# Kernel optimization log

Hardware: AMD Instinct MI355X
Metric: run time of the kernel (lower is better)

Reference implementation:

```python
import jax, jax.numpy as jnp
import numpy as np

WAY, SHOT, HEADS = 5, 5, 12
DIM, L = 768, 512
HD = DIM // HEADS  # 64
SCALE = 1.0 / (HD ** 0.5)


def _layernorm(x, g, b, eps=1e-5):
    m = jnp.mean(x, axis=-1, keepdims=True)
    v = jnp.var(x, axis=-1, keepdims=True)
    return (x - m) / jnp.sqrt(v + eps) * g + b


def setup_inputs() -> dict:
    key = jax.random.key(0)
    ks = jax.random.split(key, 7)
    x = jax.random.normal(ks[0], (WAY * SHOT, L, DIM), dtype=jnp.float32)
    Wq = 0.02 * jax.random.normal(ks[1], (DIM, DIM), dtype=jnp.float32)
    Wk = 0.02 * jax.random.normal(ks[2], (DIM, DIM), dtype=jnp.float32)
    Wv = 0.02 * jax.random.normal(ks[3], (DIM, DIM), dtype=jnp.float32)
    Wo = 0.02 * jax.random.normal(ks[4], (DIM, DIM), dtype=jnp.float32)
    wp = 0.02 * jax.random.normal(ks[5], (DIM,), dtype=jnp.float32)
    return {
        "x": x,
        "Wq": Wq, "bq": jnp.zeros((DIM,), jnp.float32),
        "Wk": Wk, "bk": jnp.zeros((DIM,), jnp.float32),
        "Wv": Wv, "bv": jnp.zeros((DIM,), jnp.float32),
        "gamma": jnp.ones((DIM,), jnp.float32),
        "beta": jnp.zeros((DIM,), jnp.float32),
        "wp": wp, "bp": jnp.zeros((), jnp.float32),
        "Wo": Wo, "bo": jnp.zeros((DIM,), jnp.float32),
    }


def reference(x, Wq, bq, Wk, bk, Wv, bv, gamma, beta, wp, bp, Wo, bo):
    # flag == 'XS' branch; mask=None; dropout in eval mode (identity).
    x = x.reshape(WAY, SHOT, L, DIM)
    # projections -> (way, heads, shot, l, head_dim)
    q = (x @ Wq.T + bq).reshape(WAY, SHOT, L, HEADS, HD).transpose(0, 3, 1, 2, 4)
    k = (x @ Wk.T + bk).reshape(WAY, SHOT, L, HEADS, HD).transpose(0, 3, 1, 2, 4)
    v = (x @ Wv.T + bv).reshape(WAY, SHOT, L, HEADS, HD).transpose(0, 3, 1, 2, 4)

    # branch 1: standard token attention, scores (w,h,s,l,l)
    s1 = jnp.einsum('whsld,whsmd->whslm', q, k) * SCALE
    w1 = jax.nn.softmax(s1, axis=-1)
    o1 = jnp.einsum('whslm,whsmd->whsld', w1, v)
    o1 = o1.transpose(0, 2, 3, 1, 4).reshape(WAY, SHOT, L, DIM)  # (w,s,l,h*d)
    a1 = jnp.max(o1, axis=2)  # max-pool over tokens -> (w,s,dim)

    # branch 2: transposed 'channel' attention across shots, scores (w,h,d,s,s)
    s2 = jnp.einsum('whsld,whtld->whdst', q, k) * SCALE
    w2 = jax.nn.softmax(s2, axis=-1)
    o2 = jnp.einsum('whdst,whtld->whdsl', w2, v)
    o2 = o2.transpose(0, 3, 4, 1, 2).reshape(WAY, SHOT, L, DIM)  # (w,s,l,h*d)
    a2 = jnp.max(o2, axis=2)  # (w,s,dim)

    attn = (_layernorm(a1, gamma, beta) + _layernorm(a2, gamma, beta)) * 0.5
    proto = jnp.tanh(attn)
    pw = jax.nn.softmax(proto @ wp + bp, axis=-1)[..., None]  # softmax over shots
    proto = pw * attn
    proto = proto @ Wo.T + bo
    return jnp.sum(proto, axis=1)  # (way, dim)
```

## Files before the change

kernel.cpp:

```cpp
#include <hip/hip_runtime.h>
#include <math.h>

#define WAY 5
#define SHOT 5
#define HEADS 12
#define DIM 768
#define LSEQ 512
#define HD 64
#define NROWS (WAY*SHOT*LSEQ)
#define SCALE 0.125f
#define NXEL ((size_t)NROWS*DIM)
#define NWEL ((size_t)DIM*DIM)

typedef __attribute__((ext_vector_type(8))) short short8;
typedef __attribute__((ext_vector_type(4))) float f32x4;
typedef __attribute__((ext_vector_type(4))) unsigned short ushort4v;

__device__ __forceinline__ float bf2f(unsigned short u) {
    union { unsigned int i; float f; } x; x.i = ((unsigned int)u) << 16; return x.f;
}
__device__ __forceinline__ unsigned short f2bf(float f) {
    union { float f; unsigned int i; } x; x.f = f;
    unsigned int r = x.i + 0x7FFFu + ((x.i >> 16) & 1u);
    return (unsigned short)(r >> 16);
}

#define NX4 (NROWS*DIM/4)
#define NW4 (DIM*DIM/4)
__global__ __launch_bounds__(256) void cast_all(
    const float* __restrict__ X, const float* __restrict__ Wq,
    const float* __restrict__ Wk, const float* __restrict__ Wv,
    unsigned short* __restrict__ Xb, unsigned short* __restrict__ Wb)
{
    int i = blockIdx.x * 256 + threadIdx.x;
    const float* s; unsigned short* d; int off;
    if (i < NX4)               { s = X;  d = Xb;            off = i; }
    else if (i < NX4 + NW4)    { s = Wq; d = Wb;            off = i - NX4; }
    else if (i < NX4 + 2*NW4)  { s = Wk; d = Wb + NWEL;     off = i - NX4 - NW4; }
    else if (i < NX4 + 3*NW4)  { s = Wv; d = Wb + 2*NWEL;   off = i - NX4 - 2*NW4; }
    else return;
    float4 f = ((const float4*)s)[off];
    ushort4v o;
    o.x = f2bf(f.x); o.y = f2bf(f.y); o.z = f2bf(f.z); o.w = f2bf(f.w);
    *(ushort4v*)(d + (size_t)off*4) = o;
}

__global__ __launch_bounds__(256) void qkv_mfma(
    const unsigned short* __restrict__ Xb, const unsigned short* __restrict__ Wball,
    const float* __restrict__ bq, const float* __restrict__ bk, const float* __restrict__ bv,
    unsigned short* __restrict__ qkv_out)
{
    const int bid  = blockIdx.x;
    const int sw   = (bid & 7) * 225 + (bid >> 3);
    const int mblk = sw / 18;
    const int nblk = sw - mblk * 18;
    const int m0   = mblk * 128;
    const int n0g  = nblk * 128;
    const int which = n0g / DIM;
    const int n0    = n0g - which * DIM;

    const unsigned short* W = Wball + (size_t)n0g * DIM;
    const float* bias = (which == 0) ? bq : ((which == 1) ? bk : bv);
    unsigned short* out = qkv_out + (size_t)which * NXEL;

    __shared__ __align__(16) unsigned short Ab[128*64];
    __shared__ __align__(16) unsigned short Bb[128*64];

    const int t = threadIdx.x;
    const int w = t >> 6;
    const int lane = t & 63;
    const int quad = lane >> 4;
    const int l15 = lane & 15;
    const int wm = (w & 1) * 64;
    const int wn = (w >> 1) * 64;

    const int srow   = lane >> 3;
    const int gchunk = (lane & 7) ^ srow;

    f32x4 acc[4][4];
    #pragma unroll
    for (int i = 0; i < 4; i++)
        #pragma unroll
        for (int j = 0; j < 4; j++)
            acc[i][j] = (f32x4){0.f, 0.f, 0.f, 0.f};

    for (int k0 = 0; k0 < DIM; k0 += 64) {
        #pragma unroll
        for (int c = 0; c < 4; c++) {
            const int lrow = w*32 + c*8;
            const unsigned short* gA = Xb + (size_t)(m0 + lrow + srow)*DIM + k0 + gchunk*8;
            const unsigned short* gB = W  + (size_t)(lrow + srow)*DIM      + k0 + gchunk*8;
            __builtin_amdgcn_global_load_lds(
                (const __attribute__((address_space(1))) unsigned int*)gA,
                (__attribute__((address_space(3))) unsigned int*)&Ab[lrow*64], 16, 0, 0);
            __builtin_amdgcn_global_load_lds(
                (const __attribute__((address_space(1))) unsigned int*)gB,
                (__attribute__((address_space(3))) unsigned int*)&Bb[lrow*64], 16, 0, 0);
        }
        __syncthreads();

        #pragma unroll
        for (int kk = 0; kk < 2; kk++) {
            const int ch = kk*4 + quad;
            short8 af[4], bf_[4];
            #pragma unroll
            for (int i = 0; i < 4; i++) {
                const int row = wm + i*16 + l15;
                af[i]  = *(const short8*)&Ab[row*64 + ((ch ^ (row & 7)) << 3)];
            }
            #pragma unroll
            for (int j = 0; j < 4; j++) {
                const int row = wn + j*16 + l15;
                bf_[j] = *(const short8*)&Bb[row*64 + ((ch ^ (row & 7)) << 3)];
            }
            #pragma unroll
            for (int i = 0; i < 4; i++)
                #pragma unroll
                for (int j = 0; j < 4; j++)
                    acc[i][j] = __builtin_amdgcn_mfma_f32_16x16x32_bf16(af[i], bf_[j], acc[i][j], 0, 0, 0);
        }
        __syncthreads();
    }

    #pragma unroll
    for (int j = 0; j < 4; j++) {
        const int col = n0 + wn + j*16 + l15;
        const float bv_ = bias[col];
        #pragma unroll
        for (int i = 0; i < 4; i++) {
            #pragma unroll
            for (int r = 0; r < 4; r++) {
                const int row = m0 + wm + i*16 + quad*4 + r;
                out[(size_t)row*DIM + col] = f2bf(acc[i][j][r] + bv_);
            }
        }
    }
}

__device__ __forceinline__ int swz(int row, int u) {
    return row*64 + ((u ^ (row & 7)) << 3);
}

__global__ __launch_bounds__(256) void attn1_mfma(
    const unsigned short* __restrict__ qb, const unsigned short* __restrict__ kb,
    const unsigned short* __restrict__ vb, float* __restrict__ a1p)
{
    int whs = blockIdx.x;
    const int chunk = blockIdx.y;
    const int si = whs % SHOT;  whs /= SHOT;
    const int hi = whs % HEADS; whs /= HEADS;
    const int wi = whs;
    const size_t baseRow = (size_t)(wi*SHOT + si) * LSEQ;
    const int colBase = hi * HD;

    __shared__ __align__(16) unsigned short Qs[64*64];
    __shared__ __align__(16) unsigned short Ks[64*64];
    __shared__ __align__(16) unsigned short Vt[64*64];
    __shared__ __align__(16) unsigned short Pb[64*64];
    __shared__ float cmaxs[4][64];

    const int t = threadIdx.x;
    const int w = t >> 6;
    const int lane = t & 63;
    const int quad = lane >> 4;
    const int l15 = lane & 15;

    #pragma unroll
    for (int p = 0; p < 2; p++) {
        int idx = p*256 + t;
        int row = idx >> 3, u = idx & 7;
        *(short8*)&Qs[swz(row, u)] =
            *(const short8*)&qb[(baseRow + chunk*64 + row)*DIM + colBase + u*8];
    }

    float l_part[4] = {0.f, 0.f, 0.f, 0.f};
    f32x4 o_acc[4];
    #pragma unroll
    for (int d = 0; d < 4; d++) o_acc[d] = (f32x4){0.f, 0.f, 0.f, 0.f};

    for (int kt = 0; kt < 8; kt++) {
        __syncthreads();
        #pragma unroll
        for (int p = 0; p < 2; p++) {
            int idx = p*256 + t;
            int row = idx >> 3, u = idx & 7;
            *(short8*)&Ks[swz(row, u)] =
                *(const short8*)&kb[(baseRow + kt*64 + row)*DIM + colBase + u*8];
        }
        #pragma unroll
        for (int p = 0; p < 2; p++) {
            int idx = p*256 + t;
            int d = idx & 63, lc = idx >> 6;
            unsigned short tmp[8];
            #pragma unroll
            for (int jj = 0; jj < 8; jj++)
                tmp[jj] = vb[(baseRow + kt*64 + lc*8 + jj)*DIM + colBase + d];
            *(short8*)&Vt[swz(d, lc)] = *(const short8*)tmp;
        }
        __syncthreads();

        f32x4 s_acc[4];
        #pragma unroll
        for (int nt = 0; nt < 4; nt++) s_acc[nt] = (f32x4){0.f, 0.f, 0.f, 0.f};
        short8 aq[2];
        #pragma unroll
        for (int kk = 0; kk < 2; kk++)
            aq[kk] = *(const short8*)&Qs[swz(w*16 + l15, kk*4 + quad)];
        #pragma unroll
        for (int kk = 0; kk < 2; kk++) {
            #pragma unroll
            for (int nt = 0; nt < 4; nt++) {
                short8 bk_ = *(const short8*)&Ks[swz(nt*16 + l15, kk*4 + quad)];
                s_acc[nt] = __builtin_amdgcn_mfma_f32_16x16x32_bf16(aq[kk], bk_, s_acc[nt], 0, 0, 0);
            }
        }

        #pragma unroll
        for (int nt = 0; nt < 4; nt++) {
            #pragma unroll
            for (int r = 0; r < 4; r++) {
                float e = __expf(s_acc[nt][r] * SCALE);
                s_acc[nt][r] = e;
                l_part[r] += e;
            }
        }

        #pragma unroll
        for (int nt = 0; nt < 4; nt++) {
            int ucol = nt*2 + (l15 >> 3);
            int cofs = l15 & 7;
            #pragma unroll
            for (int r = 0; r < 4; r++) {
                int row = w*16 + quad*4 + r;
                Pb[swz(row, ucol) + cofs] = f2bf(s_acc[nt][r]);
            }
        }

        short8 ap[2];
        #pragma unroll
        for (int kk = 0; kk < 2; kk++)
            ap[kk] = *(const short8*)&Pb[swz(w*16 + l15, kk*4 + quad)];
        #pragma unroll
        for (int kk = 0; kk < 2; kk++) {
            #pragma unroll
            for (int dt = 0; dt < 4; dt++) {
                short8 bv_ = *(const short8*)&Vt[swz(dt*16 + l15, kk*4 + quad)];
                o_acc[dt] = __builtin_amdgcn_mfma_f32_16x16x32_bf16(ap[kk], bv_, o_acc[dt], 0, 0, 0);
            }
        }
    }

    float l_tot[4];
    #pragma unroll
    for (int r = 0; r < 4; r++) {
        float s = l_part[r];
        #pragma unroll
        for (int off = 1; off < 16; off <<= 1) s += __shfl_xor(s, off);
        l_tot[r] = s;
    }

    float cm[4];
    #pragma unroll
    for (int dt = 0; dt < 4; dt++) {
        float mx = -1e30f;
        #pragma unroll
        for (int r = 0; r < 4; r++) mx = fmaxf(mx, o_acc[dt][r] / l_tot[r]);
        mx = fmaxf(mx, __shfl_xor(mx, 16));
        mx = fmaxf(mx, __shfl_xor(mx, 32));
        cm[dt] = mx;
    }
    if (quad == 0) {
        #pragma unroll
        for (int dt = 0; dt < 4; dt++) cmaxs[w][dt*16 + l15] = cm[dt];
    }
    __syncthreads();
    if (t < 64) {
        float mx = fmaxf(fmaxf(cmaxs[0][t], cmaxs[1][t]), fmaxf(cmaxs[2][t], cmaxs[3][t]));
        a1p[((size_t)((wi*HEADS + hi)*SHOT + si)*8 + chunk)*64 + t] = mx;
    }
}

__global__ __launch_bounds__(256) void attn2_scores(
    const unsigned short* __restrict__ qb, const unsigned short* __restrict__ kb,
    float* __restrict__ P1)
{
    const int wh = blockIdx.x, ch = blockIdx.y;
    const int wi = wh / HEADS, hi = wh % HEADS;
    const int t = threadIdx.x;
    const int doct = t & 7;
    const int pr = t >> 3;
    if (pr >= 25) return;
    const int si = pr / 5, tt = pr % 5;
    const int colB = hi*HD + doct*8;

    const unsigned short* qrow = qb + ((size_t)(wi*SHOT+si)*LSEQ + ch*64)*DIM + colB;
    const unsigned short* krow = kb + ((size_t)(wi*SHOT+tt)*LSEQ + ch*64)*DIM + colB;

    float acc[8] = {};
    for (int l = 0; l < 64; l++) {
        short8 q8 = *(const short8*)(qrow + (size_t)l*DIM);
        short8 k8 = *(const short8*)(krow + (size_t)l*DIM);
        #pragma unroll
        for (int j = 0; j < 8; j++)
            acc[j] += bf2f((unsigned short)q8[j]) * bf2f((unsigned short)k8[j]);
    }
    #pragma unroll
    for (int j = 0; j < 8; j++)
        P1[((size_t)(wh*25 + pr)*64 + doct*8 + j)*8 + ch] = acc[j];
}

__global__ __launch_bounds__(320) void attn2_pmax(
    const float* __restrict__ P1, const unsigned short* __restrict__ vb,
    float* __restrict__ P2)
{
    const int wh = blockIdx.x, ch = blockIdx.y;
    const int wi = wh / HEADS, hi = wh % HEADS;
    const int t = threadIdx.x;
    const int si = t / 64;
    const int r  = t & 63;
    const int doct = r >> 3, lsub = r & 7;

    __shared__ float ssc[SHOT*SHOT*HD];

    for (int e = t; e < SHOT*SHOT*HD; e += 320) {
        const float* p = P1 + (size_t)(wh*25)*64*8 + (size_t)e*8;
        float s = 0.f;
        #pragma unroll
        for (int c = 0; c < 8; c++) s += p[c];
        ssc[e] = s * SCALE;
    }
    __syncthreads();

    float wgt[SHOT][8];
    #pragma unroll
    for (int j = 0; j < 8; j++) {
        const int d = doct*8 + j;
        float sum = 0.f;
        #pragma unroll
        for (int tt = 0; tt < SHOT; tt++) {
            float e = __expf(ssc[(si*SHOT + tt)*HD + d]);
            wgt[tt][j] = e; sum += e;
        }
        const float inv = 1.f / sum;
        #pragma unroll
        for (int tt = 0; tt < SHOT; tt++) wgt[tt][j] *= inv;
    }

    const int colB = hi*HD + doct*8;
    float m[8];
    #pragma unroll
    for (int j = 0; j < 8; j++) m[j] = -1e30f;

    for (int lc = 0; lc < 8; lc++) {
        const int l = ch*64 + lsub*8 + lc;
        float val[8] = {};
        #pragma unroll
        for (int tt = 0; tt < SHOT; tt++) {
            short8 v8 = *(const short8*)(vb + ((size_t)(wi*SHOT+tt)*LSEQ + l)*DIM + colB);
            #pragma unroll
            for (int j = 0; j < 8; j++)
                val[j] += wgt[tt][j] * bf2f((unsigned short)v8[j]);
        }
        #pragma unroll
        for (int j = 0; j < 8; j++) m[j] = fmaxf(m[j], val[j]);
    }

    #pragma unroll
    for (int off = 1; off < 8; off <<= 1)
        #pragma unroll
        for (int j = 0; j < 8; j++) m[j] = fmaxf(m[j], __shfl_xor(m[j], off));

    if (lsub == 0) {
        #pragma unroll
        for (int j = 0; j < 8; j++)
            P2[((size_t)(wh*SHOT + si)*64 + doct*8 + j)*8 + ch] = m[j];
    }
}

__global__ __launch_bounds__(256) void combine(
    const float* __restrict__ a1p, const float* __restrict__ P2,
    const float* __restrict__ gamma, const float* __restrict__ beta,
    const float* __restrict__ wp, const float* __restrict__ bp,
    float* __restrict__ attn_ws, float* __restrict__ logits)
{
    const int wi = blockIdx.x / SHOT;
    const int si = blockIdx.x % SHOT;
    const int t  = threadIdx.x;

    __shared__ float row1[DIM];
    __shared__ float row2[DIM];
    __shared__ float rbuf[4][4];

    for (int j = t; j < DIM; j += 256) {
        int h = j / HD, d = j % HD;
        const float* p1 = a1p + ((size_t)((wi*HEADS + h)*SHOT + si) * 8) * 64 + d;
        float mx = -1e30f;
        #pragma unroll
        for (int c = 0; c < 8; c++) mx = fmaxf(mx, p1[c * 64]);
        row1[j] = mx;
        const float* p2 = P2 + ((size_t)((wi*HEADS + h)*SHOT + si)*64 + d)*8;
        float mx2 = -1e30f;
        #pragma unroll
        for (int c = 0; c < 8; c++) mx2 = fmaxf(mx2, p2[c]);
        row2[j] = mx2;
    }
    __syncthreads();

    float s1 = 0, q1 = 0, s2 = 0, q2 = 0;
    for (int j = t; j < DIM; j += 256) {
        float x1 = row1[j]; s1 += x1; q1 += x1*x1;
        float x2 = row2[j]; s2 += x2; q2 += x2*x2;
    }
    #pragma unroll
    for (int off = 32; off > 0; off >>= 1) {
        s1 += __shfl_down(s1, off); q1 += __shfl_down(q1, off);
        s2 += __shfl_down(s2, off); q2 += __shfl_down(q2, off);
    }
    const int wid = t / 64, lane = t % 64;
    if (lane == 0) { rbuf[wid][0] = s1; rbuf[wid][1] = q1; rbuf[wid][2] = s2; rbuf[wid][3] = q2; }
    __syncthreads();
    if (t == 0) {
        float a = 0, b = 0, c = 0, dd = 0;
        #pragma unroll
        for (int i = 0; i < 4; i++) { a += rbuf[i][0]; b += rbuf[i][1]; c += rbuf[i][2]; dd += rbuf[i][3]; }
        rbuf[0][0] = a; rbuf[0][1] = b; rbuf[0][2] = c; rbuf[0][3] = dd;
    }
    __syncthreads();
    const float mean1 = rbuf[0][0] / (float)DIM;
    const float var1  = rbuf[0][1] / (float)DIM - mean1*mean1;
    const float mean2 = rbuf[0][2] / (float)DIM;
    const float var2  = rbuf[0][3] / (float)DIM - mean2*mean2;
    const float inv1 = rsqrtf(var1 + 1e-5f);
    const float inv2 = rsqrtf(var2 + 1e-5f);

    float dotp = 0.0f;
    for (int j = t; j < DIM; j += 256) {
        float v1 = (row1[j] - mean1) * inv1 * gamma[j] + beta[j];
        float v2 = (row2[j] - mean2) * inv2 * gamma[j] + beta[j];
        float at = 0.5f * (v1 + v2);
        attn_ws[(size_t)(wi*SHOT + si) * DIM + j] = at;
        dotp += tanhf(at) * wp[j];
    }
    #pragma unroll
    for (int off = 32; off > 0; off >>= 1) dotp += __shfl_down(dotp, off);
    __syncthreads();
    if (lane == 0) rbuf[wid][0] = dotp;
    __syncthreads();
    if (t == 0)
        logits[wi*SHOT + si] = rbuf[0][0] + rbuf[1][0] + rbuf[2][0] + rbuf[3][0] + bp[0];
}

__global__ __launch_bounds__(256) void outproj(
    const float* __restrict__ attn_ws, const float* __restrict__ logits,
    const float* __restrict__ Wo, const float* __restrict__ bo,
    float* __restrict__ out)
{
    const int t = threadIdx.x;
    __shared__ __align__(16) float P[WAY][DIM];

    float swt[WAY][SHOT];
    #pragma unroll
    for (int w5 = 0; w5 < WAY; w5++) {
        float lg[SHOT];
        float mx = -1e30f;
        #pragma unroll
        for (int s = 0; s < SHOT; s++) { lg[s] = logits[w5*SHOT + s]; mx = fmaxf(mx, lg[s]); }
        float sum = 0.f;
        #pragma unroll
        for (int s = 0; s < SHOT; s++) { lg[s] = __expf(lg[s] - mx); sum += lg[s]; }
        const float inv = 1.f / sum;
        #pragma unroll
        for (int s = 0; s < SHOT; s++) swt[w5][s] = lg[s] * inv;
    }

    #pragma unroll
    for (int c = 0; c < 3; c++) {
        const int d = c*256 + t;
        #pragma unroll
        for (int w5 = 0; w5 < WAY; w5++) {
            float a = 0.f;
            #pragma unroll
            for (int s = 0; s < SHOT; s++)
                a += swt[w5][s] * attn_ws[(size_t)(w5*SHOT + s)*DIM + d];
            P[w5][d] = a;
        }
    }
    __syncthreads();

    const int wid = t >> 6, lane = t & 63;
    const int j = blockIdx.x * 4 + wid;

    float acc[WAY] = {0.f, 0.f, 0.f, 0.f, 0.f};
    #pragma unroll
    for (int c = 0; c < 3; c++) {
        const int d = c*256 + lane*4;
        const float4 wo = *(const float4*)&Wo[(size_t)j*DIM + d];
        #pragma unroll
        for (int w5 = 0; w5 < WAY; w5++) {
            const float4 p = *(const float4*)&P[w5][d];
            acc[w5] += p.x*wo.x + p.y*wo.y + p.z*wo.z + p.w*wo.w;
        }
    }
    #pragma unroll
    for (int off = 32; off > 0; off >>= 1)
        #pragma unroll
        for (int w5 = 0; w5 < WAY; w5++)
            acc[w5] += __shfl_down(acc[w5], off);

    if (lane == 0) {
        const float b5 = 5.0f * bo[j];
        #pragma unroll
        for (int w5 = 0; w5 < WAY; w5++)
            out[(size_t)w5*DIM + j] = acc[w5] + b5;
    }
}

extern "C" void kernel_launch(void* const* d_in, const int* in_sizes, int n_in,
                              void* d_out, int out_size, void* d_ws, size_t ws_size,
                              hipStream_t stream) {
    const float* X     = (const float*)d_in[0];
    const float* Wq    = (const float*)d_in[1];
    const float* bq    = (const float*)d_in[2];
    const float* Wk    = (const float*)d_in[3];
    const float* bk    = (const float*)d_in[4];
    const float* Wv    = (const float*)d_in[5];
    const float* bv    = (const float*)d_in[6];
    const float* gamma = (const float*)d_in[7];
    const float* beta  = (const float*)d_in[8];
    const float* wp    = (const float*)d_in[9];
    const float* bp    = (const float*)d_in[10];
    const float* Wo    = (const float*)d_in[11];
    const float* bo    = (const float*)d_in[12];
    float* out = (float*)d_out;

    unsigned short* Xb   = (unsigned short*)d_ws;
    unsigned short* Wb   = Xb + NXEL;
    unsigned short* qkvb = Wb + 3*NWEL;
    unsigned short* qb = qkvb;
    unsigned short* kb = qkvb + NXEL;
    unsigned short* vb = qkvb + 2*NXEL;

    float* a1p    = (float*)(qkvb + 3*NXEL);
    float* P1     = a1p + (size_t)WAY*HEADS*SHOT*8*64;
    float* P2     = P1 + (size_t)WAY*HEADS*SHOT*SHOT*64*8;
    float* attn_b = P2 + (size_t)WAY*HEADS*SHOT*64*8;
    float* logits = attn_b + (size_t)WAY*SHOT*DIM;

    const int castN = NX4 + 3*NW4;
    cast_all<<<(castN + 255)/256, 256, 0, stream>>>(X, Wq, Wk, Wv, Xb, Wb);

    qkv_mfma<<<1800, 256, 0, stream>>>(Xb, Wb, bq, bk, bv, qkvb);

    dim3 g2(WAY*HEADS*SHOT, 8);
    attn1_mfma<<<g2, 256, 0, stream>>>(qb, kb, vb, a1p);

    dim3 g3(WAY*HEADS, 8);
    attn2_scores<<<g3, 256, 0, stream>>>(qb, kb, P1);
    attn2_pmax<<<g3, 320, 0, stream>>>(P1, vb, P2);

    combine<<<WAY*SHOT, 256, 0, stream>>>(a1p, P2, gamma, beta, wp, bp, attn_b, logits);
    outproj<<<192, 256, 0, stream>>>(attn_b, logits, Wo, bo, out);
}
```

Before: 280.6 us.

## Enlarge QKV GEMM tiles to 256x256 with double-buffered LDS pipeline

```diff
diff --git a/kernel.cpp b/kernel.cpp
--- a/kernel.cpp
+++ b/kernel.cpp
@@ -45,93 +45,128 @@
     *(ushort4v*)(d + (size_t)off*4) = o;
 }
 
-__global__ __launch_bounds__(256) void qkv_mfma(
+__global__ __launch_bounds__(512, 2) void qkv_mfma(
     const unsigned short* __restrict__ Xb, const unsigned short* __restrict__ Wball,
     const float* __restrict__ bq, const float* __restrict__ bk, const float* __restrict__ bv,
     unsigned short* __restrict__ qkv_out)
 {
-    const int bid  = blockIdx.x;
-    const int sw   = (bid & 7) * 225 + (bid >> 3);
-    const int mblk = sw / 18;
-    const int nblk = sw - mblk * 18;
-    const int m0   = mblk * 128;
-    const int n0g  = nblk * 128;
-    const int which = n0g / DIM;
-    const int n0    = n0g - which * DIM;
-
-    const unsigned short* W = Wball + (size_t)n0g * DIM;
+    const int bid = blockIdx.x;
+    const int xcd = bid & 7;
+    const int loc = bid >> 3;
+    const int wgid = (xcd < 2 ? xcd*57 : 2*57 + (xcd-2)*56) + loc;
+    const int mblk = wgid / 9;
+    const int nblk = wgid % 9;
+    const int m0   = mblk * 256;
+    const int which = nblk / 3;
+    const int n0    = (nblk % 3) * 256;
+
+    const unsigned short* W = Wball + (size_t)(nblk * 256) * DIM;
     const float* bias = (which == 0) ? bq : ((which == 1) ? bk : bv);
     unsigned short* out = qkv_out + (size_t)which * NXEL;
 
-    __shared__ __align__(16) unsigned short Ab[128*64];
-    __shared__ __align__(16) unsigned short Bb[128*64];
+    __shared__ __align__(16) unsigned short Ab[2][256*64];
+    __shared__ __align__(16) unsigned short Bb[2][256*64];
 
     const int t = threadIdx.x;
     const int w = t >> 6;
     const int lane = t & 63;
     const int quad = lane >> 4;
     const int l15 = lane & 15;
-    const int wm = (w & 1) * 64;
-    const int wn = (w >> 1) * 64;
+    const int wm = w >> 2;
+    const int wn = w & 3;
 
     const int srow   = lane >> 3;
     const int gchunk = (lane & 7) ^ srow;
 
-    f32x4 acc[4][4];
-    #pragma unroll
-    for (int i = 0; i < 4; i++)
+    auto stage = [&](int kt, int buf) {
+        const int k0 = kt * 64;
+        #pragma unroll
+        for (int c = 0; c < 4; ++c) {
+            const int lrow = w*32 + c*8;
+            const unsigned short* gA = Xb + (size_t)(m0 + lrow + srow)*DIM + k0 + gchunk*8;
+            __builtin_amdgcn_global_load_lds(
+                (const __attribute__((address_space(1))) unsigned int*)gA,
+                (__attribute__((address_space(3))) unsigned int*)&Ab[buf][lrow*64], 16, 0, 0);
+            const unsigned short* gB = W + (size_t)(lrow + srow)*DIM + k0 + gchunk*8;
+            __builtin_amdgcn_global_load_lds(
+                (const __attribute__((address_space(1))) unsigned int*)gB,
+                (__attribute__((address_space(3))) unsigned int*)&Bb[buf][lrow*64], 16, 0, 0);
+        }
+    };
+
+    f32x4 acc[8][4];
+    #pragma unroll
+    for (int i = 0; i < 8; i++)
         #pragma unroll
         for (int j = 0; j < 4; j++)
             acc[i][j] = (f32x4){0.f, 0.f, 0.f, 0.f};
 
-    for (int k0 = 0; k0 < DIM; k0 += 64) {
-        #pragma unroll
-        for (int c = 0; c < 4; c++) {
-            const int lrow = w*32 + c*8;
-            const unsigned short* gA = Xb + (size_t)(m0 + lrow + srow)*DIM + k0 + gchunk*8;
-            const unsigned short* gB = W  + (size_t)(lrow + srow)*DIM      + k0 + gchunk*8;
-            __builtin_amdgcn_global_load_lds(
-                (const __attribute__((address_space(1))) unsigned int*)gA,
-                (__attribute__((address_space(3))) unsigned int*)&Ab[lrow*64], 16, 0, 0);
-            __builtin_amdgcn_global_load_lds(
-                (const __attribute__((address_space(1))) unsigned int*)gB,
-                (__attribute__((address_space(3))) unsigned int*)&Bb[lrow*64], 16, 0, 0);
-        }
-        __syncthreads();
-
-        #pragma unroll
-        for (int kk = 0; kk < 2; kk++) {
-            const int ch = kk*4 + quad;
-            short8 af[4], bf_[4];
-            #pragma unroll
-            for (int i = 0; i < 4; i++) {
-                const int row = wm + i*16 + l15;
-                af[i]  = *(const short8*)&Ab[row*64 + ((ch ^ (row & 7)) << 3)];
+    stage(0, 0);
+    stage(1, 1);
+    asm volatile("s_waitcnt vmcnt(8)" ::: "memory");
+    __builtin_amdgcn_s_barrier();
+
+    for (int kt = 0; kt < 12; ++kt) {
+        const unsigned short* As = &Ab[kt & 1][0];
+        const unsigned short* Bs = &Bb[kt & 1][0];
+
+        short8 bfr[4][2];
+        #pragma unroll
+        for (int nf = 0; nf < 4; ++nf)
+            #pragma unroll
+            for (int kk = 0; kk < 2; ++kk) {
+                const int row = wn*64 + nf*16 + l15;
+                const int ch  = kk*4 + quad;
+                bfr[nf][kk] = *(const short8*)&Bs[row*64 + ((ch ^ (row & 7)) << 3)];
             }
-            #pragma unroll
-            for (int j = 0; j < 4; j++) {
-                const int row = wn + j*16 + l15;
-                bf_[j] = *(const short8*)&Bb[row*64 + ((ch ^ (row & 7)) << 3)];
-            }
-            #pragma unroll
-            for (int i = 0; i < 4; i++)
+
+        #pragma unroll
+        for (int p = 0; p < 4; ++p) {
+            short8 afr[2][2];
+            #pragma unroll
+            for (int i = 0; i < 2; ++i)
                 #pragma unroll
-                for (int j = 0; j < 4; j++)
-                    acc[i][j] = __builtin_amdgcn_mfma_f32_16x16x32_bf16(af[i], bf_[j], acc[i][j], 0, 0, 0);
-        }
-        __syncthreads();
-    }
-
-    #pragma unroll
-    for (int j = 0; j < 4; j++) {
-        const int col = n0 + wn + j*16 + l15;
+                for (int kk = 0; kk < 2; ++kk) {
+                    const int row = wm*128 + (p*2 + i)*16 + l15;
+                    const int ch  = kk*4 + quad;
+                    afr[i][kk] = *(const short8*)&As[row*64 + ((ch ^ (row & 7)) << 3)];
+                }
+            __builtin_amdgcn_s_setprio(1);
+            #pragma unroll
+            for (int i = 0; i < 2; ++i)
+                #pragma unroll
+                for (int nf = 0; nf < 4; ++nf) {
+                    acc[p*2+i][nf] = __builtin_amdgcn_mfma_f32_16x16x32_bf16(
+                        afr[i][0], bfr[nf][0], acc[p*2+i][nf], 0, 0, 0);
+                    acc[p*2+i][nf] = __builtin_amdgcn_mfma_f32_16x16x32_bf16(
+                        afr[i][1], bfr[nf][1], acc[p*2+i][nf], 0, 0, 0);
+                }
+            __builtin_amdgcn_s_setprio(0);
+            if (p < 3) __builtin_amdgcn_s_barrier();
+        }
+
+        __builtin_amdgcn_sched_barrier(0);
+        __builtin_amdgcn_s_barrier();
+
+        if (kt + 2 < 12) {
+            stage(kt + 2, kt & 1);
+            asm volatile("s_waitcnt vmcnt(8)" ::: "memory");
+        } else {
+            asm volatile("s_waitcnt vmcnt(0)" ::: "memory");
+        }
+        __builtin_amdgcn_s_barrier();
+    }
+
+    #pragma unroll
+    for (int nf = 0; nf < 4; ++nf) {
+        const int col = n0 + wn*64 + nf*16 + l15;
         const float bv_ = bias[col];
         #pragma unroll
-        for (int i = 0; i < 4; i++) {
-            #pragma unroll
-            for (int r = 0; r < 4; r++) {
-                const int row = m0 + wm + i*16 + quad*4 + r;
-                out[(size_t)row*DIM + col] = f2bf(acc[i][j][r] + bv_);
+        for (int mf = 0; mf < 8; ++mf) {
+            #pragma unroll
+            for (int r = 0; r < 4; ++r) {
+                const int row = m0 + wm*128 + mf*16 + quad*4 + r;
+                out[(size_t)row*DIM + col] = f2bf(acc[mf][nf][r] + bv_);
             }
         }
     }
@@ -549,7 +584,7 @@
     const int castN = NX4 + 3*NW4;
     cast_all<<<(castN + 255)/256, 256, 0, stream>>>(X, Wq, Wk, Wv, Xb, Wb);
 
-    qkv_mfma<<<1800, 256, 0, stream>>>(Xb, Wb, bq, bk, bv, qkvb);
+    qkv_mfma<<<450, 512, 0, stream>>>(Xb, Wb, bq, bk, bv, qkvb);
 
     dim3 g2(WAY*HEADS*SHOT, 8);
     attn1_mfma<<<g2, 256, 0, stream>>>(qb, kb, vb, a1p);
```

Result: no change. 280.8 us (+0.1%).

## Double-buffer QKV GEMM LDS tiles and stage output through LDS

Applied to the files above, without the earlier changes.

```diff
diff --git a/kernel.cpp b/kernel.cpp
--- a/kernel.cpp
+++ b/kernel.cpp
@@ -63,8 +63,7 @@
     const float* bias = (which == 0) ? bq : ((which == 1) ? bk : bv);
     unsigned short* out = qkv_out + (size_t)which * NXEL;
 
-    __shared__ __align__(16) unsigned short Ab[128*64];
-    __shared__ __align__(16) unsigned short Bb[128*64];
+    __shared__ __align__(16) unsigned short Sm[4][128*64];
 
     const int t = threadIdx.x;
     const int w = t >> 6;
@@ -77,6 +76,9 @@
     const int srow   = lane >> 3;
     const int gchunk = (lane & 7) ^ srow;
 
+    const unsigned short* gAbase = Xb + (size_t)(m0 + w*32 + srow)*DIM + gchunk*8;
+    const unsigned short* gBbase = W  + (size_t)(w*32 + srow)*DIM      + gchunk*8;
+
     f32x4 acc[4][4];
     #pragma unroll
     for (int i = 0; i < 4; i++)
@@ -84,20 +86,32 @@
         for (int j = 0; j < 4; j++)
             acc[i][j] = (f32x4){0.f, 0.f, 0.f, 0.f};
 
-    for (int k0 = 0; k0 < DIM; k0 += 64) {
-        #pragma unroll
-        for (int c = 0; c < 4; c++) {
-            const int lrow = w*32 + c*8;
-            const unsigned short* gA = Xb + (size_t)(m0 + lrow + srow)*DIM + k0 + gchunk*8;
-            const unsigned short* gB = W  + (size_t)(lrow + srow)*DIM      + k0 + gchunk*8;
-            __builtin_amdgcn_global_load_lds(
-                (const __attribute__((address_space(1))) unsigned int*)gA,
-                (__attribute__((address_space(3))) unsigned int*)&Ab[lrow*64], 16, 0, 0);
-            __builtin_amdgcn_global_load_lds(
-                (const __attribute__((address_space(1))) unsigned int*)gB,
-                (__attribute__((address_space(3))) unsigned int*)&Bb[lrow*64], 16, 0, 0);
-        }
-        __syncthreads();
+    #define STAGE(KT, BUF)                                                        \
+        {                                                                         \
+            _Pragma("unroll")                                                     \
+            for (int c = 0; c < 4; c++) {                                         \
+                __builtin_amdgcn_global_load_lds(                                 \
+                    (const __attribute__((address_space(1))) unsigned int*)       \
+                        (gAbase + (size_t)(c*8)*DIM + (KT)*64),                   \
+                    (__attribute__((address_space(3))) unsigned int*)             \
+                        &Sm[(BUF)*2][(w*32 + c*8)*64], 16, 0, 0);                 \
+                __builtin_amdgcn_global_load_lds(                                 \
+                    (const __attribute__((address_space(1))) unsigned int*)       \
+                        (gBbase + (size_t)(c*8)*DIM + (KT)*64),                   \
+                    (__attribute__((address_space(3))) unsigned int*)             \
+                        &Sm[(BUF)*2 + 1][(w*32 + c*8)*64], 16, 0, 0);             \
+            }                                                                     \
+        }
+
+    STAGE(0, 0);
+    __syncthreads();
+
+    #pragma unroll
+    for (int kt = 0; kt < 12; ++kt) {
+        if (kt + 1 < 12) STAGE(kt + 1, (kt + 1) & 1);
+
+        const unsigned short* As = &Sm[(kt & 1) * 2][0];
+        const unsigned short* Bs = &Sm[(kt & 1) * 2 + 1][0];
 
         #pragma unroll
         for (int kk = 0; kk < 2; kk++) {
@@ -106,12 +120,12 @@
             #pragma unroll
             for (int i = 0; i < 4; i++) {
                 const int row = wm + i*16 + l15;
-                af[i]  = *(const short8*)&Ab[row*64 + ((ch ^ (row & 7)) << 3)];
+                af[i]  = *(const short8*)&As[row*64 + ((ch ^ (row & 7)) << 3)];
             }
             #pragma unroll
             for (int j = 0; j < 4; j++) {
                 const int row = wn + j*16 + l15;
-                bf_[j] = *(const short8*)&Bb[row*64 + ((ch ^ (row & 7)) << 3)];
+                bf_[j] = *(const short8*)&Bs[row*64 + ((ch ^ (row & 7)) << 3)];
             }
             #pragma unroll
             for (int i = 0; i < 4; i++)
@@ -121,19 +135,29 @@
         }
         __syncthreads();
     }
-
+    #undef STAGE
+
+    unsigned short* Cs = &Sm[0][0];
     #pragma unroll
     for (int j = 0; j < 4; j++) {
-        const int col = n0 + wn + j*16 + l15;
-        const float bv_ = bias[col];
+        const int col = wn + j*16 + l15;
+        const float bv_ = bias[n0 + col];
         #pragma unroll
         for (int i = 0; i < 4; i++) {
             #pragma unroll
             for (int r = 0; r < 4; r++) {
-                const int row = m0 + wm + i*16 + quad*4 + r;
-                out[(size_t)row*DIM + col] = f2bf(acc[i][j][r] + bv_);
-            }
-        }
+                const int row = wm + i*16 + quad*4 + r;
+                Cs[row*136 + col] = f2bf(acc[i][j][r] + bv_);
+            }
+        }
+    }
+    __syncthreads();
+    #pragma unroll
+    for (int u = 0; u < 8; u++) {
+        const int idx = u*256 + t;
+        const int row = idx >> 4, ch = idx & 15;
+        short8 v = *(const short8*)&Cs[row*136 + ch*8];
+        *(short8*)&out[(size_t)(m0 + row)*DIM + n0 + ch*8] = v;
     }
 }
 
```

Measured after the change: 265.1 us. 5.5% less time.
